# Kernel tuning notes

Hardware: AMD Instinct MI355X
Metric: run time of the kernel (lower is better)

## Reference

```python
import jax, jax.numpy as jnp
import numpy as np

B, L, D, FF = 4, 4096, 1024, 4096
EPS = 1e-06


def setup_inputs() -> dict:
    key = jax.random.key(0)
    ks = jax.random.split(key, 20)
    s_d = 1.0 / np.sqrt(D)
    s_ff = 1.0 / np.sqrt(FF)
    inp = {
        "x": jax.random.normal(ks[0], (B, L, D), jnp.float32),
        "hidden": jax.random.normal(ks[1], (B, D), jnp.float32),
        # sioconv linears (stored as [in, out])
        "w_ln_z": jax.random.normal(ks[2], (D, D), jnp.float32) * s_d,
        "b_ln_z": jnp.zeros((D,), jnp.float32),
        "w_dt": jax.random.normal(ks[3], (D, D), jnp.float32) * s_d,
        "b_dt": jnp.zeros((D,), jnp.float32),
        "w_y": jax.random.normal(ks[4], (D, D), jnp.float32) * s_d,
        "b_y": jnp.zeros((D,), jnp.float32),
        "w_y_act": jax.random.normal(ks[5], (D, D), jnp.float32) * s_d,
        "b_y_act": jnp.zeros((D,), jnp.float32),
        # FFN SwiGLU
        "w_fc": jax.random.normal(ks[6], (D, FF), jnp.float32) * s_d,
        "b_fc": jnp.zeros((FF,), jnp.float32),
        "w_fc_act": jax.random.normal(ks[7], (D, FF), jnp.float32) * s_d,
        "b_fc_act": jnp.zeros((FF,), jnp.float32),
        "w_out": jax.random.normal(ks[8], (FF, D), jnp.float32) * s_ff,
        "b_out": jnp.zeros((D,), jnp.float32),
        # RMSNorm gains
        "g_sio": jnp.ones((D,), jnp.float32),
        "g_ffn": jnp.ones((D,), jnp.float32),
    }
    return inp


def _rmsnorm(x, g):
    return x * jax.lax.rsqrt(jnp.mean(x * x, axis=-1, keepdims=True) + EPS) * g


def _sioconv(x, hidden, w_ln_z, b_ln_z, w_dt, b_dt, w_y, b_y, w_y_act, b_y_act):
    # x: [B,L,D], hidden: [B,D]
    ln_z = -jax.nn.softplus(-(x @ w_ln_z + b_ln_z))       # [B,L,D]
    dt = x @ w_dt + b_dt
    ln_da = -jax.nn.softplus(-dt)
    ln_o_da = -jax.nn.softplus(dt)
    ln_o_da_cumsum = jnp.cumsum(ln_o_da, axis=1)
    # inner-chunk: exp(logcumsumexp(ln_z + ln_da - cumsum) + cumsum)
    lse = jax.lax.cumlogsumexp(ln_z + ln_da - ln_o_da_cumsum, axis=1)
    h_inner = jnp.exp(lse + ln_o_da_cumsum)
    # cross-chunk: decay applied to incoming hidden state
    h_cross = jnp.exp(ln_o_da_cumsum) * hidden[:, None, :]
    h = h_inner + h_cross
    y = (h @ w_y + b_y) * jax.nn.silu(x @ w_y_act + b_y_act)
    return y, h


def _ffn(x, w_fc, b_fc, w_fc_act, b_fc_act, w_out, b_out):
    return (x @ w_fc + b_fc) * jax.nn.silu(x @ w_fc_act + b_fc_act) @ w_out + b_out


def reference(x, hidden, w_ln_z, b_ln_z, w_dt, b_dt, w_y, b_y, w_y_act, b_y_act,
              w_fc, b_fc, w_fc_act, b_fc_act, w_out, b_out, g_sio, g_ffn):
    x_res = x
    y, h = _sioconv(_rmsnorm(x, g_sio), hidden,
                    w_ln_z, b_ln_z, w_dt, b_dt, w_y, b_y, w_y_act, b_y_act)
    x = y + x_res  # dropout is identity (p=0 / eval)
    x_res = x
    x = _ffn(_rmsnorm(x, g_ffn), w_fc, b_fc, w_fc_act, b_fc_act, w_out, b_out) + x_res
    return (x, h)
```

## Files before the change

### kernel.cpp

```cpp
#include <hip/hip_runtime.h>
#include <stdint.h>

using u16 = unsigned short;
typedef __attribute__((ext_vector_type(8))) __bf16 bf16x8;
typedef __attribute__((ext_vector_type(4))) float f32x4;

#define DEV __device__ __forceinline__

static constexpr int kB = 4, kL = 4096, kD = 1024, kFF = 4096;
static constexpr int kM = kB * kL;
static constexpr int kLC = 64, kNC = kL / kLC;
static constexpr float kEPS = 1e-6f;

DEV u16 f2bf(float v) {
  union { float f; uint32_t u; } x; x.f = v;
  uint32_t r = x.u + 0x7FFFu + ((x.u >> 16) & 1u);
  return (u16)(r >> 16);
}
DEV float bf2f(u16 u) {
  union { uint32_t u; float f; } x; x.u = (uint32_t)u << 16; return x.f;
}
DEV float sigm(float x) { return 1.0f / (1.0f + __expf(-x)); }

DEV void gload_lds16(const void* g, void* l) {
  __builtin_amdgcn_global_load_lds(
      (const __attribute__((address_space(1))) void*)g,
      (__attribute__((address_space(3))) void*)l, 16, 0, 0);
}

__global__ __launch_bounds__(256) void wtrans_kernel(const float* __restrict__ in,
                                                     u16* __restrict__ out,
                                                     int K, int N) {
  __shared__ float t[32][33];
  const int n0 = blockIdx.x * 32, k0 = blockIdx.y * 32;
  const int tx = threadIdx.x, ty = threadIdx.y;
#pragma unroll
  for (int i = 0; i < 4; ++i)
    t[ty + i * 8][tx] = in[(size_t)(k0 + ty + i * 8) * N + (n0 + tx)];
  __syncthreads();
#pragma unroll
  for (int i = 0; i < 4; ++i)
    out[(size_t)(n0 + ty + i * 8) * K + (k0 + tx)] = f2bf(t[tx][ty + i * 8]);
}

__global__ __launch_bounds__(256) void concat_bias(const float* __restrict__ a,
                                                   const float* __restrict__ b,
                                                   float* __restrict__ o) {
  const int i = blockIdx.x * 256 + threadIdx.x;
  if (i < 1024) o[i] = a[i];
  else if (i < 2048) o[i] = b[i - 1024];
}

__global__ __launch_bounds__(256) void rmsnorm_kernel(const float* __restrict__ x,
                                                      const float* __restrict__ g,
                                                      u16* __restrict__ out) {
  const int row = blockIdx.x;
  const int t = threadIdx.x;
  const float4 v = ((const float4*)(x + (size_t)row * kD))[t];
  float ss = v.x * v.x + v.y * v.y + v.z * v.z + v.w * v.w;
#pragma unroll
  for (int o = 1; o < 64; o <<= 1) ss += __shfl_xor(ss, o, 64);
  __shared__ float red[4];
  if ((t & 63) == 0) red[t >> 6] = ss;
  __syncthreads();
  const float tot = red[0] + red[1] + red[2] + red[3];
  const float sc = rsqrtf(tot * (1.0f / kD) + kEPS);
  const float4 gv = ((const float4*)g)[t];
  const uint32_t lo = (uint32_t)f2bf(v.x * sc * gv.x) | ((uint32_t)f2bf(v.y * sc * gv.y) << 16);
  const uint32_t hi = (uint32_t)f2bf(v.z * sc * gv.z) | ((uint32_t)f2bf(v.w * sc * gv.w) << 16);
  *(uint2*)(out + (size_t)row * kD + t * 4) = make_uint2(lo, hi);
}

template <int MODE>
__global__ __launch_bounds__(512) void gemm256(
    const u16* __restrict__ A, const u16* __restrict__ Bt,
    const float* __restrict__ bias, const u16* __restrict__ aux, int auxld,
    const float* __restrict__ res, float* __restrict__ Cf,
    u16* __restrict__ Cb, float* __restrict__ C2,
    int M, int N, int K) {
  __shared__ u16 sm[65536];
  const int tid = threadIdx.x;
  const int lane = tid & 63;
  const int wave = tid >> 6;
  const int wr = wave >> 2, wc = wave & 3;

  const int gx = gridDim.x;
  const int nwg = gx * gridDim.y;
  const int bid = blockIdx.y * gx + blockIdx.x;
  const int q = nwg >> 3, r = nwg & 7;
  const int xcd = bid & 7, idx0 = bid >> 3;
  const int wg = (xcd < r ? xcd * (q + 1) : r * (q + 1) + (xcd - r) * q) + idx0;
  const int m0 = (wg / gx) * 256, n0 = (wg % gx) * 256;

  const int NK = K >> 6;

  const int l8 = lane >> 3, l7 = lane & 7;
  const int rsub = wave * 8 + l8;
  const int kel = (l7 ^ l8) * 8;
  const size_t srcA = (size_t)(m0 + rsub) * K + kel;
  const size_t srcB = (size_t)(n0 + rsub) * K + kel;

  auto stageA = [&](int kt) {
    u16* d = sm + (kt & 1) * 32768 + tid * 8;
    const u16* s = A + srcA + kt * 64;
#pragma unroll
    for (int j = 0; j < 4; ++j) gload_lds16(s + (size_t)j * 64 * K, d + j * 4096);
  };
  auto stageB = [&](int kt) {
    u16* d = sm + (kt & 1) * 32768 + 16384 + tid * 8;
    const u16* s = Bt + srcB + kt * 64;
#pragma unroll
    for (int j = 0; j < 4; ++j) gload_lds16(s + (size_t)j * 64 * K, d + j * 4096);
  };

  const int ra = lane & 15;
  const int kx0 = (((lane >> 4) ^ l7) * 8);
  const int kx1 = ((((lane >> 4) + 4) ^ l7) * 8);

  f32x4 acc[8][4] = {};
  bf16x8 a_[4][2], b_[4][2];

  stageA(0); stageB(0); stageA(1);
  asm volatile("s_waitcnt vmcnt(4)");
  asm volatile("s_barrier" ::: "memory");

  for (int h = 0; h < NK; ++h) {
    const u16* Az = sm + (h & 1) * 32768 + (wr * 128 + ra) * 64;
    const u16* Bz = sm + (h & 1) * 32768 + 16384 + (wc * 64 + ra) * 64;

#pragma unroll
    for (int mi = 0; mi < 4; ++mi) {
      a_[mi][0] = *(const bf16x8*)(Az + mi * 16 * 64 + kx0);
      a_[mi][1] = *(const bf16x8*)(Az + mi * 16 * 64 + kx1);
    }
#pragma unroll
    for (int ni = 0; ni < 2; ++ni) {
      b_[ni][0] = *(const bf16x8*)(Bz + ni * 16 * 64 + kx0);
      b_[ni][1] = *(const bf16x8*)(Bz + ni * 16 * 64 + kx1);
    }
    if (h + 1 < NK) stageB(h + 1);
    asm volatile("s_barrier" ::: "memory");
    asm volatile("s_waitcnt lgkmcnt(0)");
    __builtin_amdgcn_s_setprio(1);
#pragma unroll
    for (int mi = 0; mi < 4; ++mi)
#pragma unroll
      for (int ni = 0; ni < 2; ++ni)
#pragma unroll
        for (int kk = 0; kk < 2; ++kk)
          acc[mi][ni] = __builtin_amdgcn_mfma_f32_16x16x32_bf16(a_[mi][kk], b_[ni][kk], acc[mi][ni], 0, 0, 0);
    __builtin_amdgcn_s_setprio(0);
    asm volatile("s_barrier" ::: "memory");

#pragma unroll
    for (int ni = 0; ni < 2; ++ni) {
      b_[2 + ni][0] = *(const bf16x8*)(Bz + (32 + ni * 16) * 64 + kx0);
      b_[2 + ni][1] = *(const bf16x8*)(Bz + (32 + ni * 16) * 64 + kx1);
    }
    asm volatile("s_barrier" ::: "memory");
    asm volatile("s_waitcnt lgkmcnt(0)");
    __builtin_amdgcn_s_setprio(1);
#pragma unroll
    for (int mi = 0; mi < 4; ++mi)
#pragma unroll
      for (int ni = 0; ni < 2; ++ni)
#pragma unroll
        for (int kk = 0; kk < 2; ++kk)
          acc[mi][2 + ni] = __builtin_amdgcn_mfma_f32_16x16x32_bf16(a_[mi][kk], b_[2 + ni][kk], acc[mi][2 + ni], 0, 0, 0);
    __builtin_amdgcn_s_setprio(0);
    asm volatile("s_barrier" ::: "memory");

#pragma unroll
    for (int mi = 0; mi < 4; ++mi) {
      a_[mi][0] = *(const bf16x8*)(Az + (64 + mi * 16) * 64 + kx0);
      a_[mi][1] = *(const bf16x8*)(Az + (64 + mi * 16) * 64 + kx1);
    }
    asm volatile("s_barrier" ::: "memory");
    asm volatile("s_waitcnt lgkmcnt(0)");
    __builtin_amdgcn_s_setprio(1);
#pragma unroll
    for (int mi = 0; mi < 4; ++mi)
#pragma unroll
      for (int ni = 0; ni < 2; ++ni)
#pragma unroll
        for (int kk = 0; kk < 2; ++kk)
          acc[4 + mi][ni] = __builtin_amdgcn_mfma_f32_16x16x32_bf16(a_[mi][kk], b_[ni][kk], acc[4 + mi][ni], 0, 0, 0);
    __builtin_amdgcn_s_setprio(0);
    asm volatile("s_barrier" ::: "memory");

    if (h + 2 < NK) stageA(h + 2);
    asm volatile("s_barrier" ::: "memory");
    __builtin_amdgcn_s_setprio(1);
#pragma unroll
    for (int mi = 0; mi < 4; ++mi)
#pragma unroll
      for (int ni = 0; ni < 2; ++ni)
#pragma unroll
        for (int kk = 0; kk < 2; ++kk)
          acc[4 + mi][2 + ni] = __builtin_amdgcn_mfma_f32_16x16x32_bf16(a_[mi][kk], b_[2 + ni][kk], acc[4 + mi][2 + ni], 0, 0, 0);
    __builtin_amdgcn_s_setprio(0);
    if (h + 2 < NK) asm volatile("s_waitcnt vmcnt(4)");
    else            asm volatile("s_waitcnt vmcnt(0)");
    asm volatile("s_barrier" ::: "memory");
  }

  const int ca = ra;
  const int rq = (lane >> 4) * 4;
#pragma unroll
  for (int mi = 0; mi < 8; ++mi) {
#pragma unroll
    for (int ni = 0; ni < 4; ++ni) {
      const int c = n0 + wc * 64 + ni * 16 + ca;
      const float bz = bias[c];
#pragma unroll
      for (int j = 0; j < 4; ++j) {
        const int rr = m0 + wr * 128 + mi * 16 + rq + j;
        const size_t idx = (size_t)rr * N + c;
        const float v = acc[mi][ni][j] + bz;
        if (MODE == 1) {
          Cf[idx] = sigm(-v);
          C2[idx] = sigm(bf2f(aux[(size_t)rr * auxld + c])) * sigm(v);
        } else if (MODE == 2) {
          const float a = bf2f(aux[(size_t)rr * auxld + c]);
          Cf[idx] = v * (a * sigm(a)) + res[idx];
        } else if (MODE == 3) {
          const float a = bf2f(aux[(size_t)rr * auxld + c]);
          Cb[idx] = f2bf(v * (a * sigm(a)));
        } else if (MODE == 4) {
          Cf[idx] = v + res[idx];
        } else {
          Cb[idx] = f2bf(v);
        }
      }
    }
  }
}

__global__ __launch_bounds__(256) void scan_phase1(const float* __restrict__ Aa,
                                                   const float* __restrict__ Bv,
                                                   float* __restrict__ P,
                                                   float* __restrict__ S) {
  const int d = blockIdx.x * 256 + threadIdx.x;
  const int c = blockIdx.y, b = blockIdx.z;
  size_t base = ((size_t)b * kL + (size_t)c * kLC) * kD + d;
  float p = 1.0f, s = 0.0f;
#pragma unroll 4
  for (int l = 0; l < kLC; ++l) {
    const float a = Aa[base];
    const float bv = Bv[base];
    p *= a;
    s = fmaf(a, s, bv);
    base += kD;
  }
  const size_t o = ((size_t)b * kNC + c) * kD + d;
  P[o] = p; S[o] = s;
}

__global__ __launch_bounds__(256) void scan_phase2(const float* __restrict__ P,
                                                   const float* __restrict__ S,
                                                   const float* __restrict__ hidden,
                                                   float* __restrict__ Hini) {
  const int d = blockIdx.x * 256 + threadIdx.x;
  const int b = blockIdx.y;
  float carry = hidden[(size_t)b * kD + d];
  for (int c = 0; c < kNC; ++c) {
    const size_t o = ((size_t)b * kNC + c) * kD + d;
    Hini[o] = carry;
    carry = fmaf(P[o], carry, S[o]);
  }
}

__global__ __launch_bounds__(256) void scan_phase3(const float* __restrict__ Aa,
                                                   const float* __restrict__ Bv,
                                                   const float* __restrict__ Hini,
                                                   float* __restrict__ Hout,
                                                   u16* __restrict__ Hbf) {
  const int d = blockIdx.x * 256 + threadIdx.x;
  const int c = blockIdx.y, b = blockIdx.z;
  float h = Hini[((size_t)b * kNC + c) * kD + d];
  size_t base = ((size_t)b * kL + (size_t)c * kLC) * kD + d;
#pragma unroll 4
  for (int l = 0; l < kLC; ++l) {
    h = fmaf(Aa[base], h, Bv[base]);
    Hout[base] = h;
    Hbf[base] = f2bf(h);
    base += kD;
  }
}

extern "C" void kernel_launch(void* const* d_in, const int* in_sizes, int n_in,
                              void* d_out, int out_size, void* d_ws, size_t ws_size,
                              hipStream_t stream) {
  const float* x      = (const float*)d_in[0];
  const float* hidden = (const float*)d_in[1];
  const float* w_ln_z = (const float*)d_in[2];
  const float* b_ln_z = (const float*)d_in[3];
  const float* w_dt   = (const float*)d_in[4];
  const float* b_dt   = (const float*)d_in[5];
  const float* w_y    = (const float*)d_in[6];
  const float* b_y    = (const float*)d_in[7];
  const float* w_yact = (const float*)d_in[8];
  const float* b_yact = (const float*)d_in[9];
  const float* w_fc   = (const float*)d_in[10];
  const float* b_fc   = (const float*)d_in[11];
  const float* w_fca  = (const float*)d_in[12];
  const float* b_fca  = (const float*)d_in[13];
  const float* w_out  = (const float*)d_in[14];
  const float* b_out  = (const float*)d_in[15];
  const float* g_sio  = (const float*)d_in[16];
  const float* g_ffn  = (const float*)d_in[17];

  char* ws = (char*)d_ws;
  const size_t MiB = 1ull << 20;
  u16* wzyaT = (u16*)(ws + 0 * MiB);
  u16* wdtT  = (u16*)(ws + 4 * MiB);
  u16* wyT   = (u16*)(ws + 6 * MiB);
  u16* wfcT  = (u16*)(ws + 8 * MiB);
  u16* wfcaT = (u16*)(ws + 16 * MiB);
  u16* woutT = (u16*)(ws + 24 * MiB);
  float* bcat = (float*)(ws + 32 * MiB);
  u16*   xn   = (u16*)(ws + 33 * MiB);
  u16*   zya  = (u16*)(ws + 65 * MiB);
  float* Abuf = (float*)(ws + 129 * MiB);
  float* Bvbuf= (float*)(ws + 193 * MiB);
  u16*   hbf  = (u16*)(ws + 257 * MiB);
  float* Pbuf = (float*)(ws + 289 * MiB);
  float* Sbuf = (float*)(ws + 290 * MiB);
  float* Hini = (float*)(ws + 291 * MiB);
  u16*   Ubuf = (u16*)(ws + 193 * MiB);

  float* xout = (float*)d_out;
  float* hout = xout + (size_t)kM * kD;

  const dim3 tb(32, 8);
  wtrans_kernel<<<dim3(kD / 32, kD / 32), tb, 0, stream>>>(w_ln_z, wzyaT, kD, kD);
  wtrans_kernel<<<dim3(kD / 32, kD / 32), tb, 0, stream>>>(w_yact, wzyaT + 1024 * 1024, kD, kD);
  wtrans_kernel<<<dim3(kD / 32, kD / 32), tb, 0, stream>>>(w_dt, wdtT, kD, kD);
  wtrans_kernel<<<dim3(kD / 32, kD / 32), tb, 0, stream>>>(w_y, wyT, kD, kD);
  wtrans_kernel<<<dim3(kFF / 32, kD / 32), tb, 0, stream>>>(w_fc, wfcT, kD, kFF);
  wtrans_kernel<<<dim3(kFF / 32, kD / 32), tb, 0, stream>>>(w_fca, wfcaT, kD, kFF);
  wtrans_kernel<<<dim3(kD / 32, kFF / 32), tb, 0, stream>>>(w_out, woutT, kFF, kD);
  concat_bias<<<8, 256, 0, stream>>>(b_ln_z, b_yact, bcat);

  rmsnorm_kernel<<<kM, 256, 0, stream>>>(x, g_sio, xn);

  gemm256<5><<<dim3(2048 / 256, kM / 256), 512, 0, stream>>>(
      xn, wzyaT, bcat, nullptr, 0, nullptr, nullptr, zya, nullptr, kM, 2048, kD);
  gemm256<1><<<dim3(kD / 256, kM / 256), 512, 0, stream>>>(
      xn, wdtT, b_dt, zya, 2048, nullptr, Abuf, nullptr, Bvbuf, kM, kD, kD);

  scan_phase1<<<dim3(kD / 256, kNC, kB), 256, 0, stream>>>(Abuf, Bvbuf, Pbuf, Sbuf);
  scan_phase2<<<dim3(kD / 256, kB), 256, 0, stream>>>(Pbuf, Sbuf, hidden, Hini);
  scan_phase3<<<dim3(kD / 256, kNC, kB), 256, 0, stream>>>(Abuf, Bvbuf, Hini, hout, hbf);

  float* x1 = Abuf;
  gemm256<2><<<dim3(kD / 256, kM / 256), 512, 0, stream>>>(
      hbf, wyT, b_y, zya + 1024, 2048, x, x1, nullptr, nullptr, kM, kD, kD);

  rmsnorm_kernel<<<kM, 256, 0, stream>>>(x1, g_ffn, xn);

  for (int ci = 0; ci < 2; ++ci) {
    const int Mc = 8192;
    const u16* xc = xn + (size_t)ci * Mc * kD;
    u16* Ga = zya;
    gemm256<5><<<dim3(kFF / 256, Mc / 256), 512, 0, stream>>>(
        xc, wfcaT, b_fca, nullptr, 0, nullptr, nullptr, Ga, nullptr, Mc, kFF, kD);
    gemm256<3><<<dim3(kFF / 256, Mc / 256), 512, 0, stream>>>(
        xc, wfcT, b_fc, Ga, kFF, nullptr, nullptr, Ubuf + (size_t)ci * Mc * kFF, nullptr, Mc, kFF, kD);
  }
  gemm256<4><<<dim3(kD / 256, kM / 256), 512, 0, stream>>>(
      Ubuf, woutT, b_out, nullptr, 0, x1, xout, nullptr, nullptr, kM, kD, kFF);
}
```

Before: 821.6 us.

## Fuse gate/value GEMM pairs via interleaved weights and split LDS staging finer

Weights for ln_z/dt and fc_act/fc are interleaved in 32-column groups so a single GEMM produces both operands per tile and applies the gating epilogue directly. This removes the intermediate bf16 round-trip buffer for the gate activations and one GEMM launch per pair. The GEMM mainloop now issues global-to-LDS loads in quarter tiles spread across the MFMA phases rather than whole A/B tiles. The scan chunk length is also raised from 64 to 256, which reduces the number of chunks handled in the scan phases. Risks include added epilogue register pressure and changed scan parallelism.

```diff
diff --git a/kernel.cpp b/kernel.cpp
--- a/kernel.cpp
+++ b/kernel.cpp
@@ -9,7 +9,7 @@
 
 static constexpr int kB = 4, kL = 4096, kD = 1024, kFF = 4096;
 static constexpr int kM = kB * kL;
-static constexpr int kLC = 64, kNC = kL / kLC;
+static constexpr int kLC = 256, kNC = kL / kLC;
 static constexpr float kEPS = 1e-6f;
 
 DEV u16 f2bf(float v) {
@@ -43,12 +43,23 @@
     out[(size_t)(n0 + ty + i * 8) * K + (k0 + tx)] = f2bf(t[tx][ty + i * 8]);
 }
 
-__global__ __launch_bounds__(256) void concat_bias(const float* __restrict__ a,
+__global__ __launch_bounds__(256) void wtrans_pair(const float* __restrict__ a,
                                                    const float* __restrict__ b,
-                                                   float* __restrict__ o) {
-  const int i = blockIdx.x * 256 + threadIdx.x;
-  if (i < 1024) o[i] = a[i];
-  else if (i < 2048) o[i] = b[i - 1024];
+                                                   u16* __restrict__ out,
+                                                   int K, int Ncols) {
+  __shared__ float t[32][33];
+  const int n0 = blockIdx.x * 32, k0 = blockIdx.y * 32;
+  const int sel = (n0 >> 5) & 1;
+  const int c0 = (n0 >> 6) * 32;
+  const float* __restrict__ src = sel ? b : a;
+  const int tx = threadIdx.x, ty = threadIdx.y;
+#pragma unroll
+  for (int i = 0; i < 4; ++i)
+    t[ty + i * 8][tx] = src[(size_t)(k0 + ty + i * 8) * Ncols + (c0 + tx)];
+  __syncthreads();
+#pragma unroll
+  for (int i = 0; i < 4; ++i)
+    out[(size_t)(n0 + ty + i * 8) * K + (k0 + tx)] = f2bf(t[tx][ty + i * 8]);
 }
 
 __global__ __launch_bounds__(256) void rmsnorm_kernel(const float* __restrict__ x,
@@ -74,7 +85,8 @@
 template <int MODE>
 __global__ __launch_bounds__(512) void gemm256(
     const u16* __restrict__ A, const u16* __restrict__ Bt,
-    const float* __restrict__ bias, const u16* __restrict__ aux, int auxld,
+    const float* __restrict__ bias, const float* __restrict__ bias2,
+    const u16* __restrict__ aux, int auxld,
     const float* __restrict__ res, float* __restrict__ Cf,
     u16* __restrict__ Cb, float* __restrict__ C2,
     int M, int N, int K) {
@@ -100,28 +112,32 @@
   const size_t srcA = (size_t)(m0 + rsub) * K + kel;
   const size_t srcB = (size_t)(n0 + rsub) * K + kel;
 
-  auto stageA = [&](int kt) {
-    u16* d = sm + (kt & 1) * 32768 + tid * 8;
-    const u16* s = A + srcA + kt * 64;
-#pragma unroll
-    for (int j = 0; j < 4; ++j) gload_lds16(s + (size_t)j * 64 * K, d + j * 4096);
+  auto stage_half = [&](int kt, int half) {
+    const int bsel = (kt & 1) * 32768;
+    if (half < 2) {
+      u16* d = sm + bsel + tid * 8 + half * 8192;
+      const u16* s = A + srcA + (size_t)kt * 64 + (size_t)(half * 2) * 64 * K;
+      gload_lds16(s, d);
+      gload_lds16(s + (size_t)64 * K, d + 4096);
+    } else {
+      const int hh = half - 2;
+      u16* d = sm + bsel + 16384 + tid * 8 + hh * 8192;
+      const u16* s = Bt + srcB + (size_t)kt * 64 + (size_t)(hh * 2) * 64 * K;
+      gload_lds16(s, d);
+      gload_lds16(s + (size_t)64 * K, d + 4096);
+    }
   };
-  auto stageB = [&](int kt) {
-    u16* d = sm + (kt & 1) * 32768 + 16384 + tid * 8;
-    const u16* s = Bt + srcB + kt * 64;
-#pragma unroll
-    for (int j = 0; j < 4; ++j) gload_lds16(s + (size_t)j * 64 * K, d + j * 4096);
-  };
 
   const int ra = lane & 15;
-  const int kx0 = (((lane >> 4) ^ l7) * 8);
-  const int kx1 = ((((lane >> 4) + 4) ^ l7) * 8);
+  const int kx0 = ((lane >> 4) ^ l7) * 8;
+  const int kx1 = (((lane >> 4) + 4) ^ l7) * 8;
 
   f32x4 acc[8][4] = {};
-  bf16x8 a_[4][2], b_[4][2];
-
-  stageA(0); stageB(0); stageA(1);
-  asm volatile("s_waitcnt vmcnt(4)");
+  bf16x8 al[4][2], ah[4][2], bl[2][2], bh[2][2];
+
+  stage_half(0, 0); stage_half(0, 1); stage_half(0, 2); stage_half(0, 3);
+  stage_half(1, 0);
+  asm volatile("s_waitcnt vmcnt(2)");
   asm volatile("s_barrier" ::: "memory");
 
   for (int h = 0; h < NK; ++h) {
@@ -130,15 +146,15 @@
 
 #pragma unroll
     for (int mi = 0; mi < 4; ++mi) {
-      a_[mi][0] = *(const bf16x8*)(Az + mi * 16 * 64 + kx0);
-      a_[mi][1] = *(const bf16x8*)(Az + mi * 16 * 64 + kx1);
+      al[mi][0] = *(const bf16x8*)(Az + mi * 16 * 64 + kx0);
+      al[mi][1] = *(const bf16x8*)(Az + mi * 16 * 64 + kx1);
     }
 #pragma unroll
     for (int ni = 0; ni < 2; ++ni) {
-      b_[ni][0] = *(const bf16x8*)(Bz + ni * 16 * 64 + kx0);
-      b_[ni][1] = *(const bf16x8*)(Bz + ni * 16 * 64 + kx1);
-    }
-    if (h + 1 < NK) stageB(h + 1);
+      bl[ni][0] = *(const bf16x8*)(Bz + ni * 16 * 64 + kx0);
+      bl[ni][1] = *(const bf16x8*)(Bz + ni * 16 * 64 + kx1);
+    }
+    if (h + 1 < NK) stage_half(h + 1, 1);
     asm volatile("s_barrier" ::: "memory");
     asm volatile("s_waitcnt lgkmcnt(0)");
     __builtin_amdgcn_s_setprio(1);
@@ -148,15 +164,16 @@
       for (int ni = 0; ni < 2; ++ni)
 #pragma unroll
         for (int kk = 0; kk < 2; ++kk)
-          acc[mi][ni] = __builtin_amdgcn_mfma_f32_16x16x32_bf16(a_[mi][kk], b_[ni][kk], acc[mi][ni], 0, 0, 0);
+          acc[mi][ni] = __builtin_amdgcn_mfma_f32_16x16x32_bf16(al[mi][kk], bl[ni][kk], acc[mi][ni], 0, 0, 0);
     __builtin_amdgcn_s_setprio(0);
     asm volatile("s_barrier" ::: "memory");
 
 #pragma unroll
     for (int ni = 0; ni < 2; ++ni) {
-      b_[2 + ni][0] = *(const bf16x8*)(Bz + (32 + ni * 16) * 64 + kx0);
-      b_[2 + ni][1] = *(const bf16x8*)(Bz + (32 + ni * 16) * 64 + kx1);
-    }
+      bh[ni][0] = *(const bf16x8*)(Bz + (32 + ni * 16) * 64 + kx0);
+      bh[ni][1] = *(const bf16x8*)(Bz + (32 + ni * 16) * 64 + kx1);
+    }
+    if (h + 1 < NK) stage_half(h + 1, 2);
     asm volatile("s_barrier" ::: "memory");
     asm volatile("s_waitcnt lgkmcnt(0)");
     __builtin_amdgcn_s_setprio(1);
@@ -166,15 +183,16 @@
       for (int ni = 0; ni < 2; ++ni)
 #pragma unroll
         for (int kk = 0; kk < 2; ++kk)
-          acc[mi][2 + ni] = __builtin_amdgcn_mfma_f32_16x16x32_bf16(a_[mi][kk], b_[2 + ni][kk], acc[mi][2 + ni], 0, 0, 0);
+          acc[mi][2 + ni] = __builtin_amdgcn_mfma_f32_16x16x32_bf16(al[mi][kk], bh[ni][kk], acc[mi][2 + ni], 0, 0, 0);
     __builtin_amdgcn_s_setprio(0);
     asm volatile("s_barrier" ::: "memory");
 
 #pragma unroll
     for (int mi = 0; mi < 4; ++mi) {
-      a_[mi][0] = *(const bf16x8*)(Az + (64 + mi * 16) * 64 + kx0);
-      a_[mi][1] = *(const bf16x8*)(Az + (64 + mi * 16) * 64 + kx1);
-    }
+      ah[mi][0] = *(const bf16x8*)(Az + (64 + mi * 16) * 64 + kx0);
+      ah[mi][1] = *(const bf16x8*)(Az + (64 + mi * 16) * 64 + kx1);
+    }
+    if (h + 1 < NK) stage_half(h + 1, 3);
     asm volatile("s_barrier" ::: "memory");
     asm volatile("s_waitcnt lgkmcnt(0)");
     __builtin_amdgcn_s_setprio(1);
@@ -184,11 +202,11 @@
       for (int ni = 0; ni < 2; ++ni)
 #pragma unroll
         for (int kk = 0; kk < 2; ++kk)
-          acc[4 + mi][ni] = __builtin_amdgcn_mfma_f32_16x16x32_bf16(a_[mi][kk], b_[ni][kk], acc[4 + mi][ni], 0, 0, 0);
+          acc[4 + mi][ni] = __builtin_amdgcn_mfma_f32_16x16x32_bf16(ah[mi][kk], bl[ni][kk], acc[4 + mi][ni], 0, 0, 0);
     __builtin_amdgcn_s_setprio(0);
     asm volatile("s_barrier" ::: "memory");
 
-    if (h + 2 < NK) stageA(h + 2);
+    if (h + 2 < NK) stage_half(h + 2, 0);
     asm volatile("s_barrier" ::: "memory");
     __builtin_amdgcn_s_setprio(1);
 #pragma unroll
@@ -197,39 +215,58 @@
       for (int ni = 0; ni < 2; ++ni)
 #pragma unroll
         for (int kk = 0; kk < 2; ++kk)
-          acc[4 + mi][2 + ni] = __builtin_amdgcn_mfma_f32_16x16x32_bf16(a_[mi][kk], b_[2 + ni][kk], acc[4 + mi][2 + ni], 0, 0, 0);
+          acc[4 + mi][2 + ni] = __builtin_amdgcn_mfma_f32_16x16x32_bf16(ah[mi][kk], bh[ni][kk], acc[4 + mi][2 + ni], 0, 0, 0);
     __builtin_amdgcn_s_setprio(0);
-    if (h + 2 < NK) asm volatile("s_waitcnt vmcnt(4)");
+    if (h + 2 < NK) asm volatile("s_waitcnt vmcnt(2)");
     else            asm volatile("s_waitcnt vmcnt(0)");
     asm volatile("s_barrier" ::: "memory");
   }
 
   const int ca = ra;
   const int rq = (lane >> 4) * 4;
-#pragma unroll
-  for (int mi = 0; mi < 8; ++mi) {
-#pragma unroll
-    for (int ni = 0; ni < 4; ++ni) {
-      const int c = n0 + wc * 64 + ni * 16 + ca;
-      const float bz = bias[c];
-#pragma unroll
-      for (int j = 0; j < 4; ++j) {
-        const int rr = m0 + wr * 128 + mi * 16 + rq + j;
-        const size_t idx = (size_t)rr * N + c;
-        const float v = acc[mi][ni][j] + bz;
-        if (MODE == 1) {
-          Cf[idx] = sigm(-v);
-          C2[idx] = sigm(bf2f(aux[(size_t)rr * auxld + c])) * sigm(v);
-        } else if (MODE == 2) {
-          const float a = bf2f(aux[(size_t)rr * auxld + c]);
-          Cf[idx] = v * (a * sigm(a)) + res[idx];
-        } else if (MODE == 3) {
-          const float a = bf2f(aux[(size_t)rr * auxld + c]);
-          Cb[idx] = f2bf(v * (a * sigm(a)));
-        } else if (MODE == 4) {
-          Cf[idx] = v + res[idx];
-        } else {
-          Cb[idx] = f2bf(v);
+  if (MODE == 6 || MODE == 7) {
+    const int Nout = N >> 1;
+#pragma unroll
+    for (int mi = 0; mi < 8; ++mi) {
+#pragma unroll
+      for (int ni = 0; ni < 2; ++ni) {
+        const int cout = (n0 >> 1) + wc * 32 + ni * 16 + ca;
+        const float b1 = bias[cout], b2 = bias2[cout];
+#pragma unroll
+        for (int j = 0; j < 4; ++j) {
+          const int rr = m0 + wr * 128 + mi * 16 + rq + j;
+          const size_t idx = (size_t)rr * Nout + cout;
+          const float v1 = acc[mi][ni][j] + b1;
+          const float v2 = acc[mi][2 + ni][j] + b2;
+          if (MODE == 7) {
+            Cf[idx] = sigm(-v2);
+            C2[idx] = sigm(v1) * sigm(v2);
+          } else {
+            Cb[idx] = f2bf(v2 * (v1 * sigm(v1)));
+          }
+        }
+      }
+    }
+  } else {
+#pragma unroll
+    for (int mi = 0; mi < 8; ++mi) {
+#pragma unroll
+      for (int ni = 0; ni < 4; ++ni) {
+        const int c = n0 + wc * 64 + ni * 16 + ca;
+        const float bz = bias[c];
+#pragma unroll
+        for (int j = 0; j < 4; ++j) {
+          const int rr = m0 + wr * 128 + mi * 16 + rq + j;
+          const size_t idx = (size_t)rr * N + c;
+          const float v = acc[mi][ni][j] + bz;
+          if (MODE == 2) {
+            const float a = bf2f(aux[(size_t)rr * auxld + c]);
+            Cf[idx] = v * (a * sigm(a)) + res[idx];
+          } else if (MODE == 4) {
+            Cf[idx] = v + res[idx];
+          } else {
+            Cb[idx] = f2bf(v);
+          }
         }
       }
     }
@@ -312,62 +349,51 @@
 
   char* ws = (char*)d_ws;
   const size_t MiB = 1ull << 20;
-  u16* wzyaT = (u16*)(ws + 0 * MiB);
-  u16* wdtT  = (u16*)(ws + 4 * MiB);
+  u16* wzdT  = (u16*)(ws + 0 * MiB);
+  u16* wyaT  = (u16*)(ws + 4 * MiB);
   u16* wyT   = (u16*)(ws + 6 * MiB);
-  u16* wfcT  = (u16*)(ws + 8 * MiB);
-  u16* wfcaT = (u16*)(ws + 16 * MiB);
+  u16* wfgT  = (u16*)(ws + 8 * MiB);
   u16* woutT = (u16*)(ws + 24 * MiB);
-  float* bcat = (float*)(ws + 32 * MiB);
-  u16*   xn   = (u16*)(ws + 33 * MiB);
-  u16*   zya  = (u16*)(ws + 65 * MiB);
-  float* Abuf = (float*)(ws + 129 * MiB);
-  float* Bvbuf= (float*)(ws + 193 * MiB);
-  u16*   hbf  = (u16*)(ws + 257 * MiB);
-  float* Pbuf = (float*)(ws + 289 * MiB);
-  float* Sbuf = (float*)(ws + 290 * MiB);
-  float* Hini = (float*)(ws + 291 * MiB);
-  u16*   Ubuf = (u16*)(ws + 193 * MiB);
+  u16*   xn    = (u16*)(ws + 33 * MiB);
+  u16*   yabuf = (u16*)(ws + 65 * MiB);
+  float* Abuf  = (float*)(ws + 97 * MiB);
+  float* Bvbuf = (float*)(ws + 161 * MiB);
+  u16*   hbf   = (u16*)(ws + 225 * MiB);
+  u16*   Ubuf  = (u16*)(ws + 161 * MiB);
+  float* Pbuf  = (float*)(ws + 289 * MiB);
+  float* Sbuf  = (float*)(ws + 290 * MiB);
+  float* Hini  = (float*)(ws + 291 * MiB);
 
   float* xout = (float*)d_out;
   float* hout = xout + (size_t)kM * kD;
+  float* x1 = Abuf;
 
   const dim3 tb(32, 8);
-  wtrans_kernel<<<dim3(kD / 32, kD / 32), tb, 0, stream>>>(w_ln_z, wzyaT, kD, kD);
-  wtrans_kernel<<<dim3(kD / 32, kD / 32), tb, 0, stream>>>(w_yact, wzyaT + 1024 * 1024, kD, kD);
-  wtrans_kernel<<<dim3(kD / 32, kD / 32), tb, 0, stream>>>(w_dt, wdtT, kD, kD);
+  wtrans_pair<<<dim3(2048 / 32, kD / 32), tb, 0, stream>>>(w_ln_z, w_dt, wzdT, kD, kD);
+  wtrans_pair<<<dim3(8192 / 32, kD / 32), tb, 0, stream>>>(w_fca, w_fc, wfgT, kD, kFF);
+  wtrans_kernel<<<dim3(kD / 32, kD / 32), tb, 0, stream>>>(w_yact, wyaT, kD, kD);
   wtrans_kernel<<<dim3(kD / 32, kD / 32), tb, 0, stream>>>(w_y, wyT, kD, kD);
-  wtrans_kernel<<<dim3(kFF / 32, kD / 32), tb, 0, stream>>>(w_fc, wfcT, kD, kFF);
-  wtrans_kernel<<<dim3(kFF / 32, kD / 32), tb, 0, stream>>>(w_fca, wfcaT, kD, kFF);
   wtrans_kernel<<<dim3(kD / 32, kFF / 32), tb, 0, stream>>>(w_out, woutT, kFF, kD);
-  concat_bias<<<8, 256, 0, stream>>>(b_ln_z, b_yact, bcat);
 
   rmsnorm_kernel<<<kM, 256, 0, stream>>>(x, g_sio, xn);
 
-  gemm256<5><<<dim3(2048 / 256, kM / 256), 512, 0, stream>>>(
-      xn, wzyaT, bcat, nullptr, 0, nullptr, nullptr, zya, nullptr, kM, 2048, kD);
-  gemm256<1><<<dim3(kD / 256, kM / 256), 512, 0, stream>>>(
-      xn, wdtT, b_dt, zya, 2048, nullptr, Abuf, nullptr, Bvbuf, kM, kD, kD);
+  gemm256<7><<<dim3(2048 / 256, kM / 256), 512, 0, stream>>>(
+      xn, wzdT, b_ln_z, b_dt, nullptr, 0, nullptr, Abuf, nullptr, Bvbuf, kM, 2048, kD);
+  gemm256<5><<<dim3(kD / 256, kM / 256), 512, 0, stream>>>(
+      xn, wyaT, b_yact, nullptr, nullptr, 0, nullptr, nullptr, yabuf, nullptr, kM, kD, kD);
 
   scan_phase1<<<dim3(kD / 256, kNC, kB), 256, 0, stream>>>(Abuf, Bvbuf, Pbuf, Sbuf);
   scan_phase2<<<dim3(kD / 256, kB), 256, 0, stream>>>(Pbuf, Sbuf, hidden, Hini);
   scan_phase3<<<dim3(kD / 256, kNC, kB), 256, 0, stream>>>(Abuf, Bvbuf, Hini, hout, hbf);
 
-  float* x1 = Abuf;
   gemm256<2><<<dim3(kD / 256, kM / 256), 512, 0, stream>>>(
-      hbf, wyT, b_y, zya + 1024, 2048, x, x1, nullptr, nullptr, kM, kD, kD);
+      hbf, wyT, b_y, nullptr, yabuf, kD, x, x1, nullptr, nullptr, kM, kD, kD);
 
   rmsnorm_kernel<<<kM, 256, 0, stream>>>(x1, g_ffn, xn);
 
-  for (int ci = 0; ci < 2; ++ci) {
-    const int Mc = 8192;
-    const u16* xc = xn + (size_t)ci * Mc * kD;
-    u16* Ga = zya;
-    gemm256<5><<<dim3(kFF / 256, Mc / 256), 512, 0, stream>>>(
-        xc, wfcaT, b_fca, nullptr, 0, nullptr, nullptr, Ga, nullptr, Mc, kFF, kD);
-    gemm256<3><<<dim3(kFF / 256, Mc / 256), 512, 0, stream>>>(
-        xc, wfcT, b_fc, Ga, kFF, nullptr, nullptr, Ubuf + (size_t)ci * Mc * kFF, nullptr, Mc, kFF, kD);
-  }
+  gemm256<6><<<dim3(8192 / 256, kM / 256), 512, 0, stream>>>(
+      xn, wfgT, b_fca, b_fc, nullptr, 0, nullptr, nullptr, Ubuf, nullptr, kM, 8192, kD);
+
   gemm256<4><<<dim3(kD / 256, kM / 256), 512, 0, stream>>>(
-      Ubuf, woutT, b_out, nullptr, 0, x1, xout, nullptr, nullptr, kM, kD, kFF);
-}
+      Ubuf, woutT, b_out, nullptr, nullptr, 0, x1, xout, nullptr, nullptr, kM, kD, kFF);
+}
```

Measured after the change: 767.5 us. -6.6%, faster.
